# Performance work log

Measured on AMD Instinct MI355X. Metric: run time of the kernel, lower is better.

The kernel has to match this reference:

```python
import jax, jax.numpy as jnp
import numpy as np
from jax import lax

B, F, T = 16, 128, 4000
N_RATES = 10
EPS = 1e-05


def setup_inputs() -> dict:
    key = jax.random.key(0)
    k_x, k_s = jax.random.split(key, 2)
    x = jax.random.uniform(k_x, (B, F, T), dtype=jnp.float32)
    means = jnp.array([0.61803, 0.3904, 0.1174, 0.0606, 0.0308,
                       0.0155, 0.0078, 0.0039, 0.002, 0.0001], dtype=jnp.float32)
    # s_k ~ Normal(mean, 0.01*mean); stored as log|s_k|, shape (10, F)
    noise = jax.random.normal(k_s, (N_RATES, F), dtype=jnp.float32)
    s_log = jnp.log(jnp.abs(means[:, None] * (1.0 + 0.01 * noise)))
    alpha_log = jnp.full((F,), jnp.log(jnp.float32(0.8)), dtype=jnp.float32)
    delta_log = jnp.full((F,), jnp.log(jnp.float32(10.0)), dtype=jnp.float32)
    r_log = jnp.full((F,), jnp.log(jnp.float32(0.25)), dtype=jnp.float32)
    return {"x": x, "s_log": s_log, "alpha_log": alpha_log,
            "delta_log": delta_log, "r_log": r_log}


def reference(x, s_log, alpha_log, delta_log, r_log):
    # x: (B, F, T); s_log: (10, F); alpha/delta/r_log: (F,)
    s = jnp.exp(s_log)                      # (10, F)
    alpha = jnp.exp(alpha_log)[:, None]     # (F, 1) -> broadcast over T
    delta = jnp.exp(delta_log)[:, None]
    r = jnp.exp(r_log)[:, None]
    eps = jnp.float32(EPS)

    s_b = s[:, None, :]                     # (10, 1, F)
    init = jnp.broadcast_to(x[..., 0], (N_RATES,) + x.shape[:-1])  # (10, B, F)

    def step(carry, xt):
        # carry: (10, B, F); xt: (B, F)
        carry = (1.0 - s_b) * carry + s_b * xt
        return carry, carry

    xt_seq = jnp.moveaxis(x, -1, 0)         # (T, B, F)
    _, sm = lax.scan(step, init, xt_seq[1:])  # (T-1, 10, B, F)
    smoother = jnp.concatenate([init[None], sm], axis=0)  # (T, 10, B, F)
    smoother = jnp.moveaxis(smoother, 0, -1)               # (10, B, F, T)

    # AGC in log domain: M^(-alpha) computed as exp(-alpha*(log eps + log1p(M/eps)))
    smooth = jnp.exp(-alpha * (jnp.log(eps) + jnp.log1p(smoother / eps)))
    pcen = (x[None] * smooth + delta) ** r - delta ** r    # (10, B, F, T)
    return jnp.transpose(pcen, (1, 0, 2, 3))               # (B, 10, F, T)
```

## Files before the change

### kernel.cpp

```cpp
#include <hip/hip_runtime.h>


typedef float f32x4 __attribute__((ext_vector_type(4)));

constexpr int B_ = 16, F_ = 128, T_ = 4000, R_ = 10;
constexpr float EPS_ = 1e-5f;
constexpr int TPB = 256;
constexpr int WPB = TPB / 64;

__global__ __launch_bounds__(TPB) void pcen_kernel(
    const float* __restrict__ x,
    const float* __restrict__ s_log,
    const float* __restrict__ alpha_log,
    const float* __restrict__ delta_log,
    const float* __restrict__ r_log,
    float* __restrict__ out)
{
    const int wid  = blockIdx.x * WPB + (threadIdx.x >> 6);
    const int lane = threadIdx.x & 63;

    const int b    = wid / (R_ * F_);
    const int rem  = wid - b * (R_ * F_);
    const int rate = rem / F_;
    const int f    = rem - rate * F_;

    const float s     = __builtin_expf(s_log[rate * F_ + f]);
    const float a     = 1.0f - s;
    const float alpha = __builtin_expf(alpha_log[f]);
    const float delta = __builtin_expf(delta_log[f]);
    const float r     = __builtin_expf(r_log[f]);
    const float delta_r = __builtin_exp2f(r * __builtin_log2f(delta));

    const float a2 = a * a,     a3 = a2 * a,    a4 = a2 * a2;
    const float a5 = a4 * a,    a6 = a4 * a2,   a7 = a4 * a3,   a8 = a4 * a4;
    const float a16 = a8 * a8,  a32 = a16 * a16, a64 = a32 * a32;
    const float a128 = a64 * a64, a256 = a128 * a128;

    const float* xrow = x   + (size_t)(b * F_ + f) * T_;
    float*       orow = out + (size_t)((b * R_ + rate) * F_ + f) * T_;

    float carry = xrow[0];

    auto pcen1 = [&](float xv, float m) -> float {
        const float sm = __builtin_exp2f(-alpha * __builtin_log2f(EPS_ + m));
        return __builtin_exp2f(r * __builtin_log2f(fmaf(xv, sm, delta))) - delta_r;
    };

    for (int t0 = 0; t0 < T_; t0 += 512) {
        const int t = t0 + lane * 8;
        const bool act = (t < T_);
        float4 v0 = make_float4(0.f, 0.f, 0.f, 0.f);
        float4 v1 = make_float4(0.f, 0.f, 0.f, 0.f);
        if (act) {
            v0 = *reinterpret_cast<const float4*>(xrow + t);
            v1 = *reinterpret_cast<const float4*>(xrow + t + 4);
        }

        const float l0 = s * v0.x;
        const float l1 = fmaf(a, l0, s * v0.y);
        const float l2 = fmaf(a, l1, s * v0.z);
        const float l3 = fmaf(a, l2, s * v0.w);
        const float l4 = fmaf(a, l3, s * v1.x);
        const float l5 = fmaf(a, l4, s * v1.y);
        const float l6 = fmaf(a, l5, s * v1.z);
        const float l7 = fmaf(a, l6, s * v1.w);

        float Y = l7;
        if (lane == 0) Y = fmaf(a8, carry, Y);

        float up;
        up = __shfl_up(Y, 1);  if (lane >= 1)  Y = fmaf(a8,   up, Y);
        up = __shfl_up(Y, 2);  if (lane >= 2)  Y = fmaf(a16,  up, Y);
        up = __shfl_up(Y, 4);  if (lane >= 4)  Y = fmaf(a32,  up, Y);
        up = __shfl_up(Y, 8);  if (lane >= 8)  Y = fmaf(a64,  up, Y);
        up = __shfl_up(Y, 16); if (lane >= 16) Y = fmaf(a128, up, Y);
        up = __shfl_up(Y, 32); if (lane >= 32) Y = fmaf(a256, up, Y);

        float yin = __shfl_up(Y, 1);
        if (lane == 0) yin = carry;
        carry = __shfl(Y, 63);

        if (act) {
            const float m0 = fmaf(a,  yin, l0);
            const float m1 = fmaf(a2, yin, l1);
            const float m2 = fmaf(a3, yin, l2);
            const float m3 = fmaf(a4, yin, l3);
            const float m4 = fmaf(a5, yin, l4);
            const float m5 = fmaf(a6, yin, l5);
            const float m6 = fmaf(a7, yin, l6);
            const float m7 = fmaf(a8, yin, l7);

            f32x4 o0, o1;
            o0.x = pcen1(v0.x, m0);
            o0.y = pcen1(v0.y, m1);
            o0.z = pcen1(v0.z, m2);
            o0.w = pcen1(v0.w, m3);
            o1.x = pcen1(v1.x, m4);
            o1.y = pcen1(v1.y, m5);
            o1.z = pcen1(v1.z, m6);
            o1.w = pcen1(v1.w, m7);
            __builtin_nontemporal_store(o0, reinterpret_cast<f32x4*>(orow + t));
            __builtin_nontemporal_store(o1, reinterpret_cast<f32x4*>(orow + t + 4));
        }
    }
}

extern "C" void kernel_launch(void* const* d_in, const int* in_sizes, int n_in,
                              void* d_out, int out_size, void* d_ws, size_t ws_size,
                              hipStream_t stream) {
    const float* x         = (const float*)d_in[0];
    const float* s_log     = (const float*)d_in[1];
    const float* alpha_log = (const float*)d_in[2];
    const float* delta_log = (const float*)d_in[3];
    const float* r_log     = (const float*)d_in[4];
    float* out = (float*)d_out;

    const int n_waves = B_ * R_ * F_;
    const int blocks  = n_waves / WPB;
    pcen_kernel<<<blocks, TPB, 0, stream>>>(x, s_log, alpha_log, delta_log, r_log, out);
}
```

Baseline: 90.84 us.

## Process five smoothing rates per wave to reuse loaded input rows

Each wave now handles five rates for one (batch, frequency) row instead of one, so each x row is loaded once per five rates rather than once per rate. The per-rate coefficients and powers are forced into scalar registers with readfirstlane so they do not occupy vector registers. This cuts redundant x reads and the number of waves by a factor of five. In exchange each wave does more serial work and holds more carry state, and there is less parallelism to hide latency with.

```diff
diff --git a/kernel.cpp b/kernel.cpp
--- a/kernel.cpp
+++ b/kernel.cpp
@@ -5,8 +5,12 @@
 
 constexpr int B_ = 16, F_ = 128, T_ = 4000, R_ = 10;
 constexpr float EPS_ = 1e-5f;
-constexpr int TPB = 256;
-constexpr int WPB = TPB / 64;
+constexpr int RPW = 5, NRG = R_ / RPW;
+constexpr int TPB = 256, WPB = TPB / 64;
+
+__device__ __forceinline__ float rfl(float v) {
+    return __int_as_float(__builtin_amdgcn_readfirstlane(__float_as_int(v)));
+}
 
 __global__ __launch_bounds__(TPB) void pcen_kernel(
     const float* __restrict__ x,
@@ -19,27 +23,43 @@
     const int wid  = blockIdx.x * WPB + (threadIdx.x >> 6);
     const int lane = threadIdx.x & 63;
 
-    const int b    = wid / (R_ * F_);
-    const int rem  = wid - b * (R_ * F_);
-    const int rate = rem / F_;
-    const int f    = rem - rate * F_;
+    const int b   = wid / (NRG * F_);
+    const int rem = wid - b * (NRG * F_);
+    const int rg  = rem / F_;
+    const int f   = rem - rg * F_;
 
-    const float s     = __builtin_expf(s_log[rate * F_ + f]);
-    const float a     = 1.0f - s;
-    const float alpha = __builtin_expf(alpha_log[f]);
-    const float delta = __builtin_expf(delta_log[f]);
-    const float r     = __builtin_expf(r_log[f]);
-    const float delta_r = __builtin_exp2f(r * __builtin_log2f(delta));
+    const float alpha   = rfl(__builtin_expf(alpha_log[f]));
+    const float delta   = rfl(__builtin_expf(delta_log[f]));
+    const float r       = rfl(__builtin_expf(r_log[f]));
+    const float delta_r = rfl(__builtin_exp2f(r * __builtin_log2f(delta)));
 
-    const float a2 = a * a,     a3 = a2 * a,    a4 = a2 * a2;
-    const float a5 = a4 * a,    a6 = a4 * a2,   a7 = a4 * a3,   a8 = a4 * a4;
-    const float a16 = a8 * a8,  a32 = a16 * a16, a64 = a32 * a32;
-    const float a128 = a64 * a64, a256 = a128 * a128;
+    float sv[RPW], a1[RPW], p2[RPW], p3[RPW], p4[RPW], p5[RPW], p6[RPW], p7[RPW],
+          p8[RPW], p16[RPW], p32[RPW], p64[RPW], p128[RPW], p256[RPW];
+    float carry[RPW];
+    const float* xrow = x + (size_t)(b * F_ + f) * T_;
+    float* orow[RPW];
 
-    const float* xrow = x   + (size_t)(b * F_ + f) * T_;
-    float*       orow = out + (size_t)((b * R_ + rate) * F_ + f) * T_;
-
-    float carry = xrow[0];
+#pragma unroll
+    for (int rr = 0; rr < RPW; ++rr) {
+        const int rate = rg * RPW + rr;
+        const float s_ = rfl(__builtin_expf(s_log[rate * F_ + f]));
+        const float a_ = 1.0f - s_;
+        sv[rr] = s_;  a1[rr] = a_;
+        p2[rr]  = rfl(a_ * a_);
+        p3[rr]  = rfl(p2[rr] * a_);
+        p4[rr]  = rfl(p2[rr] * p2[rr]);
+        p5[rr]  = rfl(p4[rr] * a_);
+        p6[rr]  = rfl(p4[rr] * p2[rr]);
+        p7[rr]  = rfl(p4[rr] * p3[rr]);
+        p8[rr]  = rfl(p4[rr] * p4[rr]);
+        p16[rr] = rfl(p8[rr] * p8[rr]);
+        p32[rr] = rfl(p16[rr] * p16[rr]);
+        p64[rr] = rfl(p32[rr] * p32[rr]);
+        p128[rr] = rfl(p64[rr] * p64[rr]);
+        p256[rr] = rfl(p128[rr] * p128[rr]);
+        carry[rr] = xrow[0];
+        orow[rr]  = out + (size_t)((b * R_ + rate) * F_ + f) * T_;
+    }
 
     auto pcen1 = [&](float xv, float m) -> float {
         const float sm = __builtin_exp2f(-alpha * __builtin_log2f(EPS_ + m));
@@ -56,51 +76,56 @@
             v1 = *reinterpret_cast<const float4*>(xrow + t + 4);
         }
 
-        const float l0 = s * v0.x;
-        const float l1 = fmaf(a, l0, s * v0.y);
-        const float l2 = fmaf(a, l1, s * v0.z);
-        const float l3 = fmaf(a, l2, s * v0.w);
-        const float l4 = fmaf(a, l3, s * v1.x);
-        const float l5 = fmaf(a, l4, s * v1.y);
-        const float l6 = fmaf(a, l5, s * v1.z);
-        const float l7 = fmaf(a, l6, s * v1.w);
+#pragma unroll
+        for (int rr = 0; rr < RPW; ++rr) {
+            const float s_ = sv[rr], a_ = a1[rr];
 
-        float Y = l7;
-        if (lane == 0) Y = fmaf(a8, carry, Y);
+            const float l0 = s_ * v0.x;
+            const float l1 = fmaf(a_, l0, s_ * v0.y);
+            const float l2 = fmaf(a_, l1, s_ * v0.z);
+            const float l3 = fmaf(a_, l2, s_ * v0.w);
+            const float l4 = fmaf(a_, l3, s_ * v1.x);
+            const float l5 = fmaf(a_, l4, s_ * v1.y);
+            const float l6 = fmaf(a_, l5, s_ * v1.z);
+            const float l7 = fmaf(a_, l6, s_ * v1.w);
 
-        float up;
-        up = __shfl_up(Y, 1);  if (lane >= 1)  Y = fmaf(a8,   up, Y);
-        up = __shfl_up(Y, 2);  if (lane >= 2)  Y = fmaf(a16,  up, Y);
-        up = __shfl_up(Y, 4);  if (lane >= 4)  Y = fmaf(a32,  up, Y);
-        up = __shfl_up(Y, 8);  if (lane >= 8)  Y = fmaf(a64,  up, Y);
-        up = __shfl_up(Y, 16); if (lane >= 16) Y = fmaf(a128, up, Y);
-        up = __shfl_up(Y, 32); if (lane >= 32) Y = fmaf(a256, up, Y);
+            float Y = l7;
+            if (lane == 0) Y = fmaf(p8[rr], carry[rr], Y);
 
-        float yin = __shfl_up(Y, 1);
-        if (lane == 0) yin = carry;
-        carry = __shfl(Y, 63);
+            float up;
+            up = __shfl_up(Y, 1);  if (lane >= 1)  Y = fmaf(p8[rr],   up, Y);
+            up = __shfl_up(Y, 2);  if (lane >= 2)  Y = fmaf(p16[rr],  up, Y);
+            up = __shfl_up(Y, 4);  if (lane >= 4)  Y = fmaf(p32[rr],  up, Y);
+            up = __shfl_up(Y, 8);  if (lane >= 8)  Y = fmaf(p64[rr],  up, Y);
+            up = __shfl_up(Y, 16); if (lane >= 16) Y = fmaf(p128[rr], up, Y);
+            up = __shfl_up(Y, 32); if (lane >= 32) Y = fmaf(p256[rr], up, Y);
 
-        if (act) {
-            const float m0 = fmaf(a,  yin, l0);
-            const float m1 = fmaf(a2, yin, l1);
-            const float m2 = fmaf(a3, yin, l2);
-            const float m3 = fmaf(a4, yin, l3);
-            const float m4 = fmaf(a5, yin, l4);
-            const float m5 = fmaf(a6, yin, l5);
-            const float m6 = fmaf(a7, yin, l6);
-            const float m7 = fmaf(a8, yin, l7);
+            float yin = __shfl_up(Y, 1);
+            if (lane == 0) yin = carry[rr];
+            carry[rr] = __shfl(Y, 63);
 
-            f32x4 o0, o1;
-            o0.x = pcen1(v0.x, m0);
-            o0.y = pcen1(v0.y, m1);
-            o0.z = pcen1(v0.z, m2);
-            o0.w = pcen1(v0.w, m3);
-            o1.x = pcen1(v1.x, m4);
-            o1.y = pcen1(v1.y, m5);
-            o1.z = pcen1(v1.z, m6);
-            o1.w = pcen1(v1.w, m7);
-            __builtin_nontemporal_store(o0, reinterpret_cast<f32x4*>(orow + t));
-            __builtin_nontemporal_store(o1, reinterpret_cast<f32x4*>(orow + t + 4));
+            if (act) {
+                const float m0 = fmaf(a_,     yin, l0);
+                const float m1 = fmaf(p2[rr], yin, l1);
+                const float m2 = fmaf(p3[rr], yin, l2);
+                const float m3 = fmaf(p4[rr], yin, l3);
+                const float m4 = fmaf(p5[rr], yin, l4);
+                const float m5 = fmaf(p6[rr], yin, l5);
+                const float m6 = fmaf(p7[rr], yin, l6);
+                const float m7 = fmaf(p8[rr], yin, l7);
+
+                f32x4 o0, o1;
+                o0.x = pcen1(v0.x, m0);
+                o0.y = pcen1(v0.y, m1);
+                o0.z = pcen1(v0.z, m2);
+                o0.w = pcen1(v0.w, m3);
+                o1.x = pcen1(v1.x, m4);
+                o1.y = pcen1(v1.y, m5);
+                o1.z = pcen1(v1.z, m6);
+                o1.w = pcen1(v1.w, m7);
+                __builtin_nontemporal_store(o0, reinterpret_cast<f32x4*>(orow[rr] + t));
+                __builtin_nontemporal_store(o1, reinterpret_cast<f32x4*>(orow[rr] + t + 4));
+            }
         }
     }
 }
@@ -115,7 +140,7 @@
     const float* r_log     = (const float*)d_in[4];
     float* out = (float*)d_out;
 
-    const int n_waves = B_ * R_ * F_;
+    const int n_waves = B_ * NRG * F_;
     const int blocks  = n_waves / WPB;
     pcen_kernel<<<blocks, TPB, 0, stream>>>(x, s_log, alpha_log, delta_log, r_log, out);
 }
```

Measured after the change: 100.5 us. 1.11x slower.
